# Performance work log

Measured on AMD Instinct MI355X. Metric: run time of the kernel, lower is better.

## Reference

```python
import jax, jax.numpy as jnp
import numpy as np
from functools import lru_cache
from jax.scipy.linalg import expm

N_QUBITS = 6
DIM = 2 ** N_QUBITS          # 64
N_PAULI = 4 ** N_QUBITS      # 4096


@lru_cache(maxsize=None)
def _pauli_tensor_np(n_qubits):
    # All n-qubit Pauli strings as dense matrices, ordered base-4
    # (digit 0..3 -> I, X, Y, Z; most-significant digit = first qubit).
    I = np.eye(2, dtype=np.complex64)
    X = np.array([[0, 1], [1, 0]], dtype=np.complex64)
    Y = np.array([[0, -1j], [1j, 0]], dtype=np.complex64)
    Z = np.array([[1, 0], [0, -1]], dtype=np.complex64)
    base = np.stack([I, X, Y, Z])  # [4,2,2]
    T = base
    for _ in range(n_qubits - 1):
        k, d = T.shape[0], T.shape[1]
        T = np.einsum('iab,jcd->ijacbd', T, base).reshape(k * 4, d * 2, d * 2)
    return np.ascontiguousarray(T.astype(np.complex64))  # [4^n, 2^n, 2^n]


def setup_inputs() -> dict:
    key = jax.random.key(0)
    kx, kw, kb = jax.random.split(key, 3)
    x = jax.random.normal(kx, (512, 4000), dtype=jnp.float32)
    weight = jax.random.normal(kw, (4, N_PAULI - 1), dtype=jnp.float32)
    bias = jax.random.normal(kb, (DIM,), dtype=jnp.float32)
    return {"x": x, "weight": weight, "bias": bias}


def reference(x, weight, bias):
    # x: [B, in_dim] float32; weight: [n_reps, 4^n - 1]; bias: [out_dim]
    B, in_dim = x.shape
    n_reps = weight.shape[0]
    out_dim = bias.shape[0]
    P = jnp.asarray(_pauli_tensor_np(N_QUBITS))  # [4096, 64, 64] complex64

    # Pad data coefficients up to the full Pauli basis (identity included).
    xp = jnp.pad(x, ((0, 0), (0, N_PAULI - in_dim))).astype(jnp.complex64)

    # Data-encoding Hamiltonian per sample: H_d[b] = sum_p x[b,p] * P[p]
    Hd = jnp.einsum('bp,pij->bij', xp, P)                       # [B,64,64]
    Ud = jax.vmap(expm)(-1j * Hd)                               # [B,64,64]

    # Trainable Hamiltonians per rep (identity Pauli excluded -> global phase).
    Hp = jnp.einsum('rp,pij->rij', weight.astype(jnp.complex64), P[1:])
    Up = jax.vmap(expm)(-1j * Hp)                               # [R,64,64]

    # Data re-uploading circuit on |0...0>: repeat (U_param @ U_data).
    psi = jnp.zeros((B, DIM), dtype=jnp.complex64).at[:, 0].set(1.0)
    for r in range(n_reps):
        psi = jnp.einsum('bij,bj->bi', Ud, psi)
        psi = jnp.einsum('ij,bj->bi', Up[r], psi)

    # Observables are computational-basis projectors |k><k|, k < out_dim:
    # <psi|O_k|psi> = |psi_k|^2
    probs = (psi[:, :out_dim].real ** 2 + psi[:, :out_dim].imag ** 2)
    return probs.astype(jnp.float32) + bias
```

## Files before the change

kernel.cpp:

```cpp
#include <hip/hip_runtime.h>
#include <math.h>

typedef float2 cplx;
typedef __attribute__((ext_vector_type(8))) short short8v;
typedef __attribute__((ext_vector_type(4))) short short4v;
typedef __attribute__((ext_vector_type(4))) float float4v;

#define IN_DIM 4000
#define NREPS 4

#define C0f  1.0f
#define C1f  1.0f
#define C2f  0.5f
#define C3f  0.16666667f
#define C4f  0.041666668f
#define C5f  8.3333333e-3f
#define C6f  1.3888889e-3f
#define C7f  1.9841270e-4f
#define C8f  2.4801587e-5f
#define C9f  2.7557319e-6f
#define C10f 2.7557319e-7f
#define C11f 2.5052108e-8f
#define C12f 2.0876757e-9f
#define C13f 1.6059044e-10f
#define C14f 1.1470746e-11f
#define C15f 7.6471637e-13f

#define MFMA(A,B,C) __builtin_amdgcn_mfma_f32_16x16x32_bf16((A),(B),(C),0,0,0)


__device__ __forceinline__ int idxSw(int a, int b) {
    return (a << 6) + ((((b >> 3) + a) & 7) << 3) + (b & 7);
}
__device__ __forceinline__ short f2bf(float f) {
    unsigned u = __float_as_uint(f);
    return (short)((u + 0x7FFF + ((u >> 16) & 1)) >> 16);
}
__device__ __forceinline__ float bf2f(short s) {
    return __uint_as_float(((unsigned)(unsigned short)s) << 16);
}
__device__ __forceinline__ short8v neg8(short8v a) {
    int4 u; __builtin_memcpy(&u, &a, 16);
    u.x ^= 0x80008000; u.y ^= 0x80008000; u.z ^= 0x80008000; u.w ^= 0x80008000;
    short8v r; __builtin_memcpy(&r, &u, 16); return r;
}

template<int AM, int BM, int ND>
__device__ __forceinline__ void mm_mfma(const short* __restrict__ As,
                                        const short* __restrict__ Bs,
                                        int li, int q, int mb, int nb,
                                        float4v* __restrict__ accR,
                                        float4v* __restrict__ accI)
{
    #pragma unroll
    for (int ks = 0; ks < 2; ks++) {
        const int ch = ks * 4 + q;
        short8v arh[ND], arl[ND], cRh[ND], cRl[ND], cIh[ND], cIl[ND];
        #pragma unroll
        for (int dm = 0; dm < ND; dm++) {
            int r = ((mb + dm) << 4) + li;
            int off = (r << 6) + (((ch + r) & 7) << 3);
            arh[dm] = *(const short8v*)(As + off);
            arl[dm] = *(const short8v*)(As + 4096 + off);
            short8v aih = *(const short8v*)(As + 8192 + off);
            short8v ail = *(const short8v*)(As + 12288 + off);
            short8v nih = neg8(aih), nil_ = neg8(ail);
            cRh[dm] = (AM == 2) ? aih : nih;
            cRl[dm] = (AM == 2) ? ail : nil_;
            cIh[dm] = (AM == 2) ? nih : aih;
            cIl[dm] = (AM == 2) ? nil_ : ail;
        }
        #pragma unroll
        for (int dn = 0; dn < ND; dn++) {
            int n = ((nb + dn) << 4) + li;
            int off = (n << 6) + (((ch + n) & 7) << 3);
            short8v brh = *(const short8v*)(Bs + off);
            short8v brl = *(const short8v*)(Bs + 4096 + off);
            short8v bih = *(const short8v*)(Bs + 8192 + off);
            short8v bil = *(const short8v*)(Bs + 12288 + off);
            if (BM == 1) { brh = neg8(brh); brl = neg8(brl); }
            #pragma unroll
            for (int dm = 0; dm < ND; dm++) {
                int ti = dm * ND + dn;
                accR[ti] = MFMA(arh[dm], brh, accR[ti]);
                accR[ti] = MFMA(arh[dm], brl, accR[ti]);
                accR[ti] = MFMA(arl[dm], brh, accR[ti]);
                accR[ti] = MFMA(cRh[dm], bih, accR[ti]);
                accR[ti] = MFMA(cRh[dm], bil, accR[ti]);
                accR[ti] = MFMA(cRl[dm], bih, accR[ti]);
                accI[ti] = MFMA(arh[dm], bih, accI[ti]);
                accI[ti] = MFMA(arh[dm], bil, accI[ti]);
                accI[ti] = MFMA(arl[dm], bih, accI[ti]);
                accI[ti] = MFMA(cIh[dm], brh, accI[ti]);
                accI[ti] = MFMA(cIh[dm], brl, accI[ti]);
                accI[ti] = MFMA(cIl[dm], brh, accI[ti]);
            }
        }
    }
}

template<int ND>
__device__ __forceinline__ void write_row(short* __restrict__ S, int li, int q,
                                          int mb, int nb,
                                          const float4v* cre, const float4v* cim)
{
    #pragma unroll
    for (int dm = 0; dm < ND; dm++)
    #pragma unroll
    for (int dn = 0; dn < ND; dn++) {
        int ti = dm * ND + dn;
        int c = ((nb + dn) << 4) + li;
        #pragma unroll
        for (int reg = 0; reg < 4; reg++) {
            int r = ((mb + dm) << 4) + q * 4 + reg;
            int off = idxSw(r, c);
            float vr = cre[ti][reg], vi = cim[ti][reg];
            short rh = f2bf(vr), rl = f2bf(vr - bf2f(rh));
            short ih = f2bf(vi), il = f2bf(vi - bf2f(ih));
            S[off] = rh; S[4096 + off] = rl; S[8192 + off] = ih; S[12288 + off] = il;
        }
    }
}

template<int ND>
__device__ __forceinline__ void write_rowT(short* __restrict__ S, int li, int q,
                                           int mb, int nb,
                                           const float4v* cre, const float4v* cim)
{
    #pragma unroll
    for (int dm = 0; dm < ND; dm++)
    #pragma unroll
    for (int dn = 0; dn < ND; dn++) {
        int ti = dm * ND + dn;
        int c = ((nb + dn) << 4) + li;
        int k0 = ((mb + dm) << 4) + q * 4;
        int off = idxSw(c, k0);
        short4v rh, rl, ih, il;
        #pragma unroll
        for (int reg = 0; reg < 4; reg++) {
            float vr = cre[ti][reg], vi = cim[ti][reg];
            short h1 = f2bf(vr); rh[reg] = h1; rl[reg] = f2bf(vr - bf2f(h1));
            short h2 = f2bf(vi); ih[reg] = h2; il[reg] = f2bf(vi - bf2f(h2));
        }
        *(short4v*)(S + off) = rh;
        *(short4v*)(S + 4096 + off) = rl;
        *(short4v*)(S + 8192 + off) = ih;
        *(short4v*)(S + 12288 + off) = il;
    }
}

template<int ND>
__device__ __forceinline__ void gather_tile(const short* __restrict__ S, int li, int q,
                                            int mb, int nb, float4v* bre, float4v* bim)
{
    #pragma unroll
    for (int dm = 0; dm < ND; dm++)
    #pragma unroll
    for (int dn = 0; dn < ND; dn++) {
        int ti = dm * ND + dn;
        int c = ((nb + dn) << 4) + li;
        #pragma unroll
        for (int reg = 0; reg < 4; reg++) {
            int r = ((mb + dm) << 4) + q * 4 + reg;
            int off = idxSw(r, c);
            bre[ti][reg] = bf2f(S[off]) + bf2f(S[4096 + off]);
            bim[ti][reg] = bf2f(S[8192 + off]) + bf2f(S[12288 + off]);
        }
    }
}

template<int ND>
__device__ __forceinline__ void adddiag(float4v* u, float cI, int li, int q, int mb, int nb)
{
    #pragma unroll
    for (int dm = 0; dm < ND; dm++)
    #pragma unroll
    for (int dn = 0; dn < ND; dn++) {
        if (mb + dm == nb + dn) {
            #pragma unroll
            for (int e = 0; e < 4; e++)
                if (li == q * 4 + e) u[dm * ND + dn][e] += cI;
        }
    }
}

template<int ND>
__device__ __forceinline__ void store_tiles(cplx* __restrict__ dst, int li, int q,
                                            int mb, int nb,
                                            const float4v* ure, const float4v* uim)
{
    #pragma unroll
    for (int dm = 0; dm < ND; dm++)
    #pragma unroll
    for (int dn = 0; dn < ND; dn++) {
        int ti = dm * ND + dn;
        int c = ((nb + dn) << 4) + li;
        int cs = c ^ (((c >> 4) & 1) << 1);
        #pragma unroll
        for (int reg = 0; reg < 4; reg++) {
            int r = ((mb + dm) << 4) + q * 4 + reg;
            dst[(r << 6) + cs] = make_float2(ure[ti][reg], uim[ti][reg]);
        }
    }
}

__device__ __forceinline__ cplx pauli_phase(float v, int xm, int zm) {
    int ny = __popc(xm & zm) & 3;
    if (ny == 0) return make_float2(v, 0.f);
    if (ny == 1) return make_float2(0.f, -v);
    if (ny == 2) return make_float2(-v, 0.f);
    return make_float2(0.f, v);
}

template<int WPB>
__device__ __forceinline__ void expm_core(char* __restrict__ LDS,
                                          const float* __restrict__ src, bool isW,
                                          int t, float4v* ure, float4v* uim)
{
    constexpr int ND    = (WPB == 4) ? 2 : 1;
    constexpr int NT    = ND * ND;
    constexpr int TPBv  = WPB * 64;
    constexpr int LITER = 4096 / TPBv;
    constexpr int ROWS  = 64 / WPB;
    constexpr int L4    = (WPB == 4) ? 4 : 5;
    short* S0 = (short*)LDS;
    short* S1 = (short*)(LDS + 32768);
    cplx*  W  = (cplx*)(LDS + 32768);
    float* red = (float*)(LDS + 65536);
    const int lane = t & 63, wv = t >> 6;
    const int li = lane & 15, q = lane >> 4;
    const int mb = (WPB == 4) ? ((wv & 1) << 1) : (wv & 3);
    const int nb = (WPB == 4) ? ((wv >> 1) << 1) : (wv >> 2);

    int xmt = 0, zmt = 0;
    #pragma unroll
    for (int k = 0; k < 6; k++) {
        int lo = (t >> (2 * k)) & 1, hi = (t >> (2 * k + 1)) & 1;
        zmt |= hi << k; xmt |= (hi ^ lo) << k;
    }
    float sumsq = 0.f;
    #pragma unroll
    for (int n = 0; n < LITER; n++) {
        int p = t + TPBv * n;
        int lo0 = n & 1, hi0 = (n >> 1) & 1, lo1 = (n >> 2) & 1, hi1 = (n >> 3) & 1;
        int zmn = hi0 | (hi1 << 1), xmn = (hi0 ^ lo0) | ((hi1 ^ lo1) << 1);
        int xm = xmt | (xmn << L4), zm = zmt | (zmn << L4);
        float v = isW ? ((p == 0) ? 0.f : src[p - 1])
                      : ((p < IN_DIM) ? src[p] : 0.f);
        sumsq += v * v;
        W[(xm << 6) + zm] = pauli_phase(v, xm, zm);
    }
    #pragma unroll
    for (int d = 32; d >= 1; d >>= 1) sumsq += __shfl_xor(sumsq, d, 64);
    if (lane == 0) red[wv] = sumsq;
    __syncthreads();

    float rs = 0.f;
    #pragma unroll
    for (int i2 = 0; i2 < WPB; i2++) rs += red[i2];
    float fro = sqrtf(64.f * rs);
    int s1 = 0; { float nn = fro; while (nn > 8.f && s1 < 24) { nn *= 0.5f; s1++; } }
    float sc1 = exp2f((float)(-s1));

    cplx hv[ROWS];
    #pragma unroll
    for (int rr = 0; rr < ROWS; rr++) hv[rr] = W[((wv * ROWS + rr) << 6) + lane];
    #pragma unroll
    for (int d = 1; d < 64; d <<= 1) {
        float sg = (lane & d) ? -1.f : 1.f;
        #pragma unroll
        for (int rr = 0; rr < ROWS; rr++) {
            float px = __shfl_xor(hv[rr].x, d, 64);
            float py = __shfl_xor(hv[rr].y, d, 64);
            hv[rr].x = fmaf(sg, hv[rr].x, px);
            hv[rr].y = fmaf(sg, hv[rr].y, py);
        }
    }

    #pragma unroll
    for (int rr = 0; rr < ROWS; rr++) {
        int m = wv * ROWS + rr;
        int c = lane ^ m;
        float vr = hv[rr].y * sc1, vi = -hv[rr].x * sc1;
        short rh = f2bf(vr), rl = f2bf(vr - bf2f(rh));
        short ih = f2bf(vi), il = f2bf(vi - bf2f(ih));
        int off = idxSw(lane, c);
        S0[off] = rh; S0[4096 + off] = rl; S0[8192 + off] = ih; S0[12288 + off] = il;
    }
    __syncthreads();

    const float4v z4 = {0.f, 0.f, 0.f, 0.f};
    float4v accR[NT], accI[NT];
    #define ZERO_ACC _Pragma("unroll") for (int i2 = 0; i2 < NT; i2++) { accR[i2]=z4; accI[i2]=z4; }

    ZERO_ACC
    mm_mfma<0, 1, ND>(S0, S0, li, q, mb, nb, accR, accI);
    float ss = 0.f;
    #pragma unroll
    for (int ti = 0; ti < NT; ti++)
        #pragma unroll
        for (int e = 0; e < 4; e++)
            ss += accR[ti][e]*accR[ti][e] + accI[ti][e]*accI[ti][e];
    #pragma unroll
    for (int d = 32; d >= 1; d >>= 1) ss += __shfl_xor(ss, d, 64);
    if (lane == 0) red[WPB + wv] = ss;
    __syncthreads();

    rs = 0.f;
    #pragma unroll
    for (int i2 = 0; i2 < WPB; i2++) rs += red[WPB + i2];
    float bound = sqrtf(sqrtf(rs));
    int ds = 0; { float nn = bound; while (nn > 3.4f && ds < 12) { nn *= 0.5f; ds++; } }
    const int s = s1 + ds;
    float dsc = exp2f((float)(-ds)), dsc2 = dsc * dsc;

    float4v bre[NT], bim[NT];
    gather_tile<ND>(S0, li, q, mb, nb, bre, bim);

    #pragma unroll
    for (int ti = 0; ti < NT; ti++) { ure[ti] = accR[ti] * dsc2; uim[ti] = accI[ti] * dsc2; }
    write_rowT<ND>(S1, li, q, mb, nb, ure, uim);
    __syncthreads();

    {
        float ca = C15f * dsc;
        #pragma unroll
        for (int ti = 0; ti < NT; ti++) { ure[ti] = ca * bre[ti]; uim[ti] = ca * bim[ti]; }
        adddiag<ND>(ure, C14f, li, q, mb, nb);
        write_rowT<ND>(S0, li, q, mb, nb, ure, uim);
    }
    __syncthreads();

    const float cIc[7] = { C0f, C2f, C4f, C6f, C8f, C10f, C12f };
    const float cAc[7] = { C1f, C3f, C5f, C7f, C9f, C11f, C13f };
    for (int j = 6; j >= 0; j--) {
        ZERO_ACC
        mm_mfma<2, 0, ND>(S1, S0, li, q, mb, nb, accR, accI);
        __syncthreads();
        float ca = cAc[j] * dsc, cI = cIc[j];
        #pragma unroll
        for (int ti = 0; ti < NT; ti++) {
            ure[ti] = accR[ti] + ca * bre[ti];
            uim[ti] = accI[ti] + ca * bim[ti];
        }
        adddiag<ND>(ure, cI, li, q, mb, nb);
        write_rowT<ND>(S0, li, q, mb, nb, ure, uim);
        __syncthreads();
    }

    for (int sq = 0; sq < s; sq++) {
        write_row<ND>(S1, li, q, mb, nb, ure, uim);
        if (sq > 0) write_rowT<ND>(S0, li, q, mb, nb, ure, uim);
        __syncthreads();
        ZERO_ACC
        mm_mfma<0, 0, ND>(S1, S0, li, q, mb, nb, accR, accI);
        __syncthreads();
        #pragma unroll
        for (int ti = 0; ti < NT; ti++) { ure[ti] = accR[ti]; uim[ti] = accI[ti]; }
    }
    #undef ZERO_ACC
}

__device__ __forceinline__ cplx matvec_wave(const cplx* __restrict__ M,
                                            const cplx* __restrict__ pin,
                                            int lane, int wv)
{
    const int rr = (wv << 4) + (lane & 15);
    const int kc = lane >> 4;
    float ax = 0.f, ay = 0.f;
    const float4* Mr = (const float4*)(M + (rr << 6));
    #pragma unroll
    for (int c = 0; c < 4; c++) {
        int ch = ((kc << 2) + c + rr) & 15;
        int b = (ch >> 2) & 1;
        float4 m01 = Mr[(ch << 1) + b];
        float4 m23 = Mr[(ch << 1) + 1 - b];
        const cplx* p = pin + (ch << 2);
        cplx p0 = p[0], p1 = p[1], p2 = p[2], p3 = p[3];
        ax = fmaf(m01.x, p0.x, fmaf(-m01.y, p0.y, ax));
        ay = fmaf(m01.x, p0.y, fmaf( m01.y, p0.x, ay));
        ax = fmaf(m01.z, p1.x, fmaf(-m01.w, p1.y, ax));
        ay = fmaf(m01.z, p1.y, fmaf( m01.w, p1.x, ay));
        ax = fmaf(m23.x, p2.x, fmaf(-m23.y, p2.y, ax));
        ay = fmaf(m23.x, p2.y, fmaf( m23.y, p2.x, ay));
        ax = fmaf(m23.z, p3.x, fmaf(-m23.w, p3.y, ax));
        ay = fmaf(m23.z, p3.y, fmaf( m23.w, p3.x, ay));
    }
    ax += __shfl_xor(ax, 16, 64); ay += __shfl_xor(ay, 16, 64);
    ax += __shfl_xor(ax, 32, 64); ay += __shfl_xor(ay, 32, 64);
    return make_float2(ax, ay);
}

__global__ __launch_bounds__(1024) void up_kernel(const float* __restrict__ w,
                                                  cplx* __restrict__ ws)
{
    __shared__ float4 LDSf4[4104];
    char* LDS = (char*)LDSf4;
    const int t = threadIdx.x, r = blockIdx.x;
    float4v ure[1], uim[1];
    expm_core<16>(LDS, w + (size_t)r * 4095, true, t, ure, uim);

    const int lane = t & 63, wv = t >> 6, li = lane & 15, q = lane >> 4;
    store_tiles<1>(ws + ((size_t)r << 12), li, q, wv & 3, wv >> 2, ure, uim);
}

__global__ __launch_bounds__(256) void circuit_kernel(const float* __restrict__ x,
                                                      const cplx* __restrict__ ws,
                                                      const float* __restrict__ bias,
                                                      float* __restrict__ out)
{
    __shared__ float4 LDSf4[4168];
    char* LDS = (char*)LDSf4;
    const int t = threadIdx.x, b = blockIdx.x;
    float4v ure[4], uim[4];
    expm_core<4>(LDS, x + (size_t)b * IN_DIM, false, t, ure, uim);

    cplx* Ud   = (cplx*)(LDS + 32768);
    cplx* UpS  = (cplx*)LDS;
    cplx* psiA = (cplx*)(LDS + 65664);
    cplx* psiB = (cplx*)(LDS + 66176);

    const int lane = t & 63, wv = t >> 6, li = lane & 15, q = lane >> 4;
    store_tiles<2>(Ud, li, q, (wv & 1) << 1, (wv >> 1) << 1, ure, uim);
    if (t < 64) psiA[t] = make_float2(t == 0 ? 1.f : 0.f, 0.f);
    __syncthreads();

    const int rowi = (wv << 4) + (lane & 15);
    for (int r = 0; r < NREPS; r++) {
        {
            const float4* srcv = (const float4*)(ws + ((size_t)r << 12));
            float4* dstY = (float4*)UpS;
            #pragma unroll
            for (int n = 0; n < 8; n++) dstY[n * 256 + t] = srcv[n * 256 + t];
        }
        cplx v1 = matvec_wave(Ud, psiA, lane, wv);
        if (lane < 16) psiB[rowi] = v1;
        __syncthreads();
        cplx v2 = matvec_wave(UpS, psiB, lane, wv);
        if (lane < 16) psiA[rowi] = v2;
        __syncthreads();
    }
    if (t < 64) {
        cplx pv = psiA[t];
        out[(b << 6) + t] = fmaf(pv.x, pv.x, fmaf(pv.y, pv.y, bias[t]));
    }
}

extern "C" void kernel_launch(void* const* d_in, const int* in_sizes, int n_in,
                              void* d_out, int out_size, void* d_ws, size_t ws_size,
                              hipStream_t stream)
{
    const float* x    = (const float*)d_in[0];
    const float* w    = (const float*)d_in[1];
    const float* bias = (const float*)d_in[2];
    float* out = (float*)d_out;
    cplx* ws   = (cplx*)d_ws;

    int B = in_sizes[0] / IN_DIM;

    hipLaunchKernelGGL(up_kernel,      dim3(NREPS), dim3(1024), 0, stream, w, ws);
    hipLaunchKernelGGL(circuit_kernel, dim3(B),     dim3(256),  0, stream, x, ws, bias, out);
}
```

Measured before the change: 154.9 us.

## Fuse Up expm into circuit kernel with flag sync and Paterson-Stockmeyer Taylor

Removes the separate up_kernel launch. The first NREPS blocks of the circuit kernel compute the parameter unitaries, publish them to workspace and signal through an atomic counter. Every block spin-waits on that counter before its matvec loop. The Taylor polynomial evaluation is restructured to precompute A^2 and A^3 and use a Paterson-Stockmeyer-style Horner scheme, which cuts the number of 64x64 matmuls from about 8 to 5. This adds an inter-block spin wait, which depends on the first blocks being resident, plus a memset launch, and changes launch bounds to request 2 blocks per CU.

```diff
diff --git a/kernel.cpp b/kernel.cpp
--- a/kernel.cpp
+++ b/kernel.cpp
@@ -212,25 +212,18 @@
     return make_float2(0.f, v);
 }
 
-template<int WPB>
-__device__ __forceinline__ void expm_core(char* __restrict__ LDS,
-                                          const float* __restrict__ src, bool isW,
-                                          int t, float4v* ure, float4v* uim)
-{
-    constexpr int ND    = (WPB == 4) ? 2 : 1;
-    constexpr int NT    = ND * ND;
-    constexpr int TPBv  = WPB * 64;
-    constexpr int LITER = 4096 / TPBv;
-    constexpr int ROWS  = 64 / WPB;
-    constexpr int L4    = (WPB == 4) ? 4 : 5;
+__device__ __forceinline__ void expm_core4(char* __restrict__ LDS,
+                                           const float* __restrict__ src, bool isW,
+                                           int t, float4v* ure, float4v* uim)
+{
+    constexpr int ND = 2, NT = 4;
     short* S0 = (short*)LDS;
     short* S1 = (short*)(LDS + 32768);
     cplx*  W  = (cplx*)(LDS + 32768);
     float* red = (float*)(LDS + 65536);
     const int lane = t & 63, wv = t >> 6;
     const int li = lane & 15, q = lane >> 4;
-    const int mb = (WPB == 4) ? ((wv & 1) << 1) : (wv & 3);
-    const int nb = (WPB == 4) ? ((wv >> 1) << 1) : (wv >> 2);
+    const int mb = (wv & 1) << 1, nb = (wv >> 1) << 1;
 
     int xmt = 0, zmt = 0;
     #pragma unroll
@@ -240,11 +233,11 @@
     }
     float sumsq = 0.f;
     #pragma unroll
-    for (int n = 0; n < LITER; n++) {
-        int p = t + TPBv * n;
+    for (int n = 0; n < 16; n++) {
+        int p = t + 256 * n;
         int lo0 = n & 1, hi0 = (n >> 1) & 1, lo1 = (n >> 2) & 1, hi1 = (n >> 3) & 1;
         int zmn = hi0 | (hi1 << 1), xmn = (hi0 ^ lo0) | ((hi1 ^ lo1) << 1);
-        int xm = xmt | (xmn << L4), zm = zmt | (zmn << L4);
+        int xm = xmt | (xmn << 4), zm = zmt | (zmn << 4);
         float v = isW ? ((p == 0) ? 0.f : src[p - 1])
                       : ((p < IN_DIM) ? src[p] : 0.f);
         sumsq += v * v;
@@ -257,19 +250,19 @@
 
     float rs = 0.f;
     #pragma unroll
-    for (int i2 = 0; i2 < WPB; i2++) rs += red[i2];
+    for (int i2 = 0; i2 < 4; i2++) rs += red[i2];
     float fro = sqrtf(64.f * rs);
     int s1 = 0; { float nn = fro; while (nn > 8.f && s1 < 24) { nn *= 0.5f; s1++; } }
     float sc1 = exp2f((float)(-s1));
 
-    cplx hv[ROWS];
-    #pragma unroll
-    for (int rr = 0; rr < ROWS; rr++) hv[rr] = W[((wv * ROWS + rr) << 6) + lane];
+    cplx hv[16];
+    #pragma unroll
+    for (int rr = 0; rr < 16; rr++) hv[rr] = W[((wv * 16 + rr) << 6) + lane];
     #pragma unroll
     for (int d = 1; d < 64; d <<= 1) {
         float sg = (lane & d) ? -1.f : 1.f;
         #pragma unroll
-        for (int rr = 0; rr < ROWS; rr++) {
+        for (int rr = 0; rr < 16; rr++) {
             float px = __shfl_xor(hv[rr].x, d, 64);
             float py = __shfl_xor(hv[rr].y, d, 64);
             hv[rr].x = fmaf(sg, hv[rr].x, px);
@@ -278,8 +271,8 @@
     }
 
     #pragma unroll
-    for (int rr = 0; rr < ROWS; rr++) {
-        int m = wv * ROWS + rr;
+    for (int rr = 0; rr < 16; rr++) {
+        int m = wv * 16 + rr;
         int c = lane ^ m;
         float vr = hv[rr].y * sc1, vi = -hv[rr].x * sc1;
         short rh = f2bf(vr), rl = f2bf(vr - bf2f(rh));
@@ -303,12 +296,12 @@
             ss += accR[ti][e]*accR[ti][e] + accI[ti][e]*accI[ti][e];
     #pragma unroll
     for (int d = 32; d >= 1; d >>= 1) ss += __shfl_xor(ss, d, 64);
-    if (lane == 0) red[WPB + wv] = ss;
+    if (lane == 0) red[4 + wv] = ss;
     __syncthreads();
 
     rs = 0.f;
     #pragma unroll
-    for (int i2 = 0; i2 < WPB; i2++) rs += red[WPB + i2];
+    for (int i2 = 0; i2 < 4; i2++) rs += red[4 + i2];
     float bound = sqrtf(sqrtf(rs));
     int ds = 0; { float nn = bound; while (nn > 3.4f && ds < 12) { nn *= 0.5f; ds++; } }
     const int s = s1 + ds;
@@ -316,42 +309,59 @@
 
     float4v bre[NT], bim[NT];
     gather_tile<ND>(S0, li, q, mb, nb, bre, bim);
-
-    #pragma unroll
-    for (int ti = 0; ti < NT; ti++) { ure[ti] = accR[ti] * dsc2; uim[ti] = accI[ti] * dsc2; }
-    write_rowT<ND>(S1, li, q, mb, nb, ure, uim);
-    __syncthreads();
-
+    float4v a2r[NT], a2i[NT];
+    #pragma unroll
+    for (int ti = 0; ti < NT; ti++) { a2r[ti] = accR[ti] * dsc2; a2i[ti] = accI[ti] * dsc2; }
+    write_rowT<ND>(S1, li, q, mb, nb, a2r, a2i);
+    __syncthreads();
+
+    ZERO_ACC
+    mm_mfma<2, 1, ND>(S1, S0, li, q, mb, nb, accR, accI);
+    float4v a3r[NT], a3i[NT];
+    #pragma unroll
+    for (int ti = 0; ti < NT; ti++) { a3r[ti] = accR[ti] * dsc; a3i[ti] = accI[ti] * dsc; }
+    ZERO_ACC
+    mm_mfma<2, 0, ND>(S1, S1, li, q, mb, nb, accR, accI);
+    __syncthreads();
+    write_rowT<ND>(S0, li, q, mb, nb, accR, accI);
     {
-        float ca = C15f * dsc;
-        #pragma unroll
-        for (int ti = 0; ti < NT; ti++) { ure[ti] = ca * bre[ti]; uim[ti] = ca * bim[ti]; }
-        adddiag<ND>(ure, C14f, li, q, mb, nb);
-        write_rowT<ND>(S0, li, q, mb, nb, ure, uim);
-    }
-    __syncthreads();
-
-    const float cIc[7] = { C0f, C2f, C4f, C6f, C8f, C10f, C12f };
-    const float cAc[7] = { C1f, C3f, C5f, C7f, C9f, C11f, C13f };
-    for (int j = 6; j >= 0; j--) {
+        float caA = C13f * dsc, ca3 = C15f * dsc;
+        #pragma unroll
+        for (int ti = 0; ti < NT; ti++) {
+            ure[ti] = caA * bre[ti] + C14f * a2r[ti] + ca3 * a3r[ti];
+            uim[ti] = caA * bim[ti] + C14f * a2i[ti] + ca3 * a3i[ti];
+        }
+        adddiag<ND>(ure, C12f, li, q, mb, nb);
+        write_row<ND>(S1, li, q, mb, nb, ure, uim);
+    }
+    __syncthreads();
+
+    const float cIc[3] = { C0f, C4f, C8f };
+    const float cAc[3] = { C1f, C5f, C9f };
+    const float c2c[3] = { C2f, C6f, C10f };
+    const float c3c[3] = { C3f, C7f, C11f };
+    for (int j = 2; j >= 0; j--) {
         ZERO_ACC
-        mm_mfma<2, 0, ND>(S1, S0, li, q, mb, nb, accR, accI);
-        __syncthreads();
-        float ca = cAc[j] * dsc, cI = cIc[j];
+        mm_mfma<0, 0, ND>(S1, S0, li, q, mb, nb, accR, accI);
+        __syncthreads();
+        float caA = cAc[j] * dsc, ca3 = c3c[j] * dsc;
         #pragma unroll
         for (int ti = 0; ti < NT; ti++) {
-            ure[ti] = accR[ti] + ca * bre[ti];
-            uim[ti] = accI[ti] + ca * bim[ti];
-        }
-        adddiag<ND>(ure, cI, li, q, mb, nb);
-        write_rowT<ND>(S0, li, q, mb, nb, ure, uim);
+            ure[ti] = accR[ti] + caA * bre[ti] + c2c[j] * a2r[ti] + ca3 * a3r[ti];
+            uim[ti] = accI[ti] + caA * bim[ti] + c2c[j] * a2i[ti] + ca3 * a3i[ti];
+        }
+        adddiag<ND>(ure, cIc[j], li, q, mb, nb);
+        write_row<ND>(S1, li, q, mb, nb, ure, uim);
+        if (j == 0) write_rowT<ND>(S0, li, q, mb, nb, ure, uim);
         __syncthreads();
     }
 
     for (int sq = 0; sq < s; sq++) {
-        write_row<ND>(S1, li, q, mb, nb, ure, uim);
-        if (sq > 0) write_rowT<ND>(S0, li, q, mb, nb, ure, uim);
-        __syncthreads();
+        if (sq > 0) {
+            write_row<ND>(S1, li, q, mb, nb, ure, uim);
+            write_rowT<ND>(S0, li, q, mb, nb, ure, uim);
+            __syncthreads();
+        }
         ZERO_ACC
         mm_mfma<0, 0, ND>(S1, S0, li, q, mb, nb, accR, accI);
         __syncthreads();
@@ -391,38 +401,41 @@
     return make_float2(ax, ay);
 }
 
-__global__ __launch_bounds__(1024) void up_kernel(const float* __restrict__ w,
-                                                  cplx* __restrict__ ws)
-{
-    __shared__ float4 LDSf4[4104];
-    char* LDS = (char*)LDSf4;
-    const int t = threadIdx.x, r = blockIdx.x;
-    float4v ure[1], uim[1];
-    expm_core<16>(LDS, w + (size_t)r * 4095, true, t, ure, uim);
-
-    const int lane = t & 63, wv = t >> 6, li = lane & 15, q = lane >> 4;
-    store_tiles<1>(ws + ((size_t)r << 12), li, q, wv & 3, wv >> 2, ure, uim);
-}
-
-__global__ __launch_bounds__(256) void circuit_kernel(const float* __restrict__ x,
-                                                      const cplx* __restrict__ ws,
-                                                      const float* __restrict__ bias,
-                                                      float* __restrict__ out)
+__global__ __launch_bounds__(256, 2) void circuit_kernel(const float* __restrict__ x,
+                                                         const float* __restrict__ w,
+                                                         const float* __restrict__ bias,
+                                                         cplx* __restrict__ ws,
+                                                         int* __restrict__ flag,
+                                                         float* __restrict__ out)
 {
     __shared__ float4 LDSf4[4168];
     char* LDS = (char*)LDSf4;
     const int t = threadIdx.x, b = blockIdx.x;
+    const int lane = t & 63, wv = t >> 6, li = lane & 15, q = lane >> 4;
     float4v ure[4], uim[4];
-    expm_core<4>(LDS, x + (size_t)b * IN_DIM, false, t, ure, uim);
+
+    if (b < NREPS) {
+        expm_core4(LDS, w + (size_t)b * 4095, true, t, ure, uim);
+        store_tiles<2>(ws + ((size_t)b << 12), li, q, (wv & 1) << 1, (wv >> 1) << 1,
+                       ure, uim);
+        __syncthreads();
+        if (t == 0)
+            __hip_atomic_fetch_add(flag, 1, __ATOMIC_RELEASE, __HIP_MEMORY_SCOPE_AGENT);
+    }
+
+    expm_core4(LDS, x + (size_t)b * IN_DIM, false, t, ure, uim);
 
     cplx* Ud   = (cplx*)(LDS + 32768);
     cplx* UpS  = (cplx*)LDS;
     cplx* psiA = (cplx*)(LDS + 65664);
     cplx* psiB = (cplx*)(LDS + 66176);
 
-    const int lane = t & 63, wv = t >> 6, li = lane & 15, q = lane >> 4;
     store_tiles<2>(Ud, li, q, (wv & 1) << 1, (wv >> 1) << 1, ure, uim);
     if (t < 64) psiA[t] = make_float2(t == 0 ? 1.f : 0.f, 0.f);
+    if (t == 0) {
+        while (__hip_atomic_load(flag, __ATOMIC_ACQUIRE, __HIP_MEMORY_SCOPE_AGENT) < NREPS)
+            __builtin_amdgcn_s_sleep(8);
+    }
     __syncthreads();
 
     const int rowi = (wv << 4) + (lane & 15);
@@ -455,9 +468,11 @@
     const float* bias = (const float*)d_in[2];
     float* out = (float*)d_out;
     cplx* ws   = (cplx*)d_ws;
+    int* flag  = (int*)((char*)d_ws + (NREPS << 15));
 
     int B = in_sizes[0] / IN_DIM;
 
-    hipLaunchKernelGGL(up_kernel,      dim3(NREPS), dim3(1024), 0, stream, w, ws);
-    hipLaunchKernelGGL(circuit_kernel, dim3(B),     dim3(256),  0, stream, x, ws, bias, out);
-}
+    hipMemsetAsync(flag, 0, sizeof(int), stream);
+    hipLaunchKernelGGL(circuit_kernel, dim3(B), dim3(256), 0, stream,
+                       x, w, bias, ws, flag, out);
+}
```

New measurement: 166.6 us. 7.6% more time.
